# Kernel optimization log

Measured on AMD Instinct MI355X. Metric: run time of the kernel, lower is better.

## Reference

```python
import jax, jax.numpy as jnp
import numpy as np

N_WIRES = 8
N_LAYERS = 6
OUTPUT_DIM = 8
BATCH = 131072


def _rx(t):
    c = jnp.cos(t / 2).astype(jnp.complex64)
    s = jnp.sin(t / 2).astype(jnp.complex64)
    return jnp.stack([jnp.stack([c, -1j * s], -1), jnp.stack([-1j * s, c], -1)], -2)


def _ry(t):
    c = jnp.cos(t / 2).astype(jnp.complex64)
    s = jnp.sin(t / 2).astype(jnp.complex64)
    return jnp.stack([jnp.stack([c, -s], -1), jnp.stack([s, c], -1)], -2)


def _rz(t):
    e = jnp.exp(-0.5j * t.astype(jnp.complex64))
    z = jnp.zeros_like(e)
    return jnp.stack([jnp.stack([e, z], -1), jnp.stack([z, jnp.conj(e)], -1)], -2)


def _apply_1q(state, U, w):
    # state: [B, 2, 2, ..., 2]; U: [2,2] (shared) or [B,2,2] (per-batch angle)
    s = jnp.moveaxis(state, w + 1, -1)
    if U.ndim == 3:
        s = jnp.einsum('bij,b...j->b...i', U, s)
    else:
        s = jnp.einsum('ij,...j->...i', U, s)
    return jnp.moveaxis(s, -1, w + 1)


def _apply_cnot(state, c, t):
    s = jnp.moveaxis(state, (c + 1, t + 1), (-2, -1))
    s = jnp.concatenate([s[..., :1, :], s[..., 1:, ::-1]], axis=-2)
    return jnp.moveaxis(s, (-2, -1), (c + 1, t + 1))


def _circuit(x, weights):
    B = x.shape[0]
    dim = 2 ** N_WIRES
    state = jnp.zeros((B, dim), dtype=jnp.complex64).at[:, 0].set(1.0)
    state = state.reshape((B,) + (2,) * N_WIRES)
    rx0 = _rx(x[:, 0])  # [B,2,2] data-encoding gates (batched angles)
    ry1 = _ry(x[:, 1])
    for layer in range(N_LAYERS):
        for i in range(N_WIRES):
            state = _apply_1q(state, rx0 if i % 2 == 0 else ry1, i)
        for i in range(N_WIRES):
            state = _apply_1q(state, _rx(weights[layer, i, 0]), i)
            state = _apply_1q(state, _ry(weights[layer, i, 1]), i)
            state = _apply_1q(state, _rz(weights[layer, i, 2]), i)
        for i in range(N_WIRES - 1):
            state = _apply_cnot(state, i, i + 1)
    probs = state.real ** 2 + state.imag ** 2  # [B, 2,...,2]
    evs = []
    for i in range(OUTPUT_DIM):
        p = jnp.moveaxis(probs, i + 1, 1).reshape(B, 2, -1)
        evs.append((p[:, 0] - p[:, 1]).sum(-1))  # <Z_i>
    return jnp.stack(evs, 0)  # [output_dim, B]


def setup_inputs() -> dict:
    key = jax.random.key(0)
    k1, k2 = jax.random.split(key)
    x = jax.random.normal(k1, (BATCH, 2), dtype=jnp.float32)
    weights = jax.random.normal(k2, (N_LAYERS, N_WIRES, 3), dtype=jnp.float32)
    return {'x': x, 'weights': weights}


def reference(x, weights):
    basis_t = _circuit(x, weights) * jnp.pi  # [output_dim, B]
    return basis_t.T  # [B, output_dim]
```

## Files before the change

### kernel.cpp

```cpp
#include <hip/hip_runtime.h>
#include <math.h>

#define N_WIRES 8
#define N_LAYERS 6
#define NG 49
#define NG2 (NG * NG)

#define WS_E_OFF 0
#define WS_FB_OFF 76832

typedef _Float16 half8 __attribute__((ext_vector_type(8)));
typedef float f32x4 __attribute__((ext_vector_type(4)));

__global__ __launch_bounds__(256) void qnn_grid_lds(const float* __restrict__ w,
                                                    float* __restrict__ E) {
    __shared__ float gates[N_LAYERS * N_WIRES * 8];
    __shared__ float2 amps[256];
    __shared__ float partial[4][8];

    const int tid = threadIdx.x;
    const int g = blockIdx.x;
    const int ga = (g * 1338) >> 16;
    const int gb = g - ga * NG;
    const float step = (float)(2.0 * M_PI / 49.0);

    if (tid < N_LAYERS * N_WIRES) {
        const int i = tid & 7;
        float wx = w[tid * 3 + 0], wy = w[tid * 3 + 1], wz = w[tid * 3 + 2];
        float sx, cx, sy, cy, sz, cz;
        sincosf(0.5f * wx, &sx, &cx);
        sincosf(0.5f * wy, &sy, &cy);
        sincosf(0.5f * wz, &sz, &cz);
        float A00r = cy * cx, A00i = sy * sx;
        float A01r = -sy * cx, A01i = -cy * sx;
        float A10r = sy * cx, A10i = -cy * sx;
        float A11r = cy * cx, A11i = -sy * sx;
        float U00r = A00r * cz + A00i * sz, U00i = A00i * cz - A00r * sz;
        float U01r = A01r * cz + A01i * sz, U01i = A01i * cz - A01r * sz;
        float U10r = A10r * cz - A10i * sz, U10i = A10i * cz + A10r * sz;
        float U11r = A11r * cz - A11i * sz, U11i = A11i * cz + A11r * sz;
        float V00r, V00i, V01r, V01i, V10r, V10i, V11r, V11i;
        if ((i & 1) == 0) {
            V00r = U01i; V00i = -U01r;
            V01r = U00i; V01i = -U00r;
            V10r = U11i; V10i = -U11r;
            V11r = U10i; V11i = -U10r;
        } else {
            V00r = U01r;  V00i = U01i;
            V01r = -U00r; V01i = -U00i;
            V10r = U11r;  V10i = U11i;
            V11r = -U10r; V11i = -U10i;
        }
        const float xx = (i & 1) ? (step * (float)gb) : (step * (float)ga);
        float se, ce;
        sincosf(0.5f * xx, &se, &ce);
        float* o = gates + tid * 8;
        o[0] = ce * U00r + se * V00r;  o[1] = ce * U00i + se * V00i;
        o[2] = ce * U01r + se * V01r;  o[3] = ce * U01i + se * V01i;
        o[4] = ce * U10r + se * V10r;  o[5] = ce * U10i + se * V10i;
        o[6] = ce * U11r + se * V11r;  o[7] = ce * U11i + se * V11i;
    }

    float ar = (tid == 0) ? 1.0f : 0.0f;
    float ai = 0.0f;
    __syncthreads();

    for (int l = 0; l < N_LAYERS; ++l) {
        #pragma unroll
        for (int i = 0; i < 8; ++i) {
            const float* gm = gates + (l * 8 + i) * 8;
            const int p = 7 - i;
            const int m = 1 << p;
            const int bit = (tid >> p) & 1;
            amps[tid] = make_float2(ar, ai);
            __syncthreads();
            float2 other = amps[tid ^ m];
            float a0r = bit ? other.x : ar, a0i = bit ? other.y : ai;
            float a1r = bit ? ar : other.x, a1i = bit ? ai : other.y;
            float c0r = gm[bit * 4 + 0], c0i = gm[bit * 4 + 1];
            float c1r = gm[bit * 4 + 2], c1i = gm[bit * 4 + 3];
            float nr = c0r * a0r - c0i * a0i + c1r * a1r - c1i * a1i;
            float ni = c0r * a0i + c0i * a0r + c1r * a1i + c1i * a1r;
            __syncthreads();
            ar = nr; ai = ni;
        }
        amps[tid] = make_float2(ar, ai);
        __syncthreads();
        float2 src = amps[tid ^ (tid >> 1)];
        ar = src.x; ai = src.y;
        __syncthreads();
    }

    float p = ar * ar + ai * ai;
    float ev[8];
    #pragma unroll
    for (int i = 0; i < 8; ++i) ev[i] = ((tid >> (7 - i)) & 1) ? -p : p;
    #pragma unroll
    for (int i = 0; i < 8; ++i) {
        #pragma unroll
        for (int s = 1; s < 64; s <<= 1) ev[i] += __shfl_xor(ev[i], s);
    }
    const int wave = tid >> 6, lane = tid & 63;
    if (lane == 0) {
        #pragma unroll
        for (int i = 0; i < 8; ++i) partial[wave][i] = ev[i];
    }
    __syncthreads();
    if (tid < 8) {
        E[tid * NG2 + g] = partial[0][tid] + partial[1][tid] + partial[2][tid] + partial[3][tid];
    }
}

__global__ __launch_bounds__(64) void dft2(const float* __restrict__ E,
                                           _Float16* __restrict__ Fb) {
    const int kp = blockIdx.x, i = blockIdx.y, t = threadIdx.x;
    __shared__ float Es[NG2];
    __shared__ float H[NG];
    const float step = (float)(2.0 * M_PI / 49.0);

    if (kp < NG) {
        for (int e = t; e < NG2; e += 64) Es[e] = E[i * NG2 + e];
    }
    __syncthreads();

    if (kp < NG && t < NG) {
        const int b = t;
        float acc = 0.f;
        if (kp == 0) {
            for (int a = 0; a < NG; ++a) acc += Es[a * NG + b];
            acc *= (1.0f / 49.0f);
        } else {
            const int n = (kp + 1) >> 1;
            float cs, ss;
            sincosf(step * (float)n, &ss, &cs);
            float ca = 1.f, sa = 0.f;
            const bool use_cos = (kp & 1);
            for (int a = 0; a < NG; ++a) {
                acc = fmaf(Es[a * NG + b], use_cos ? ca : sa, acc);
                float cn = ca * cs - sa * ss;
                float sn = sa * cs + ca * ss;
                ca = cn; sa = sn;
            }
            acc *= (2.0f / 49.0f);
        }
        H[b] = acc;
    }
    __syncthreads();

    const int l = t;
    const float PI = 3.14159265358979323846f;
    float acc = 0.f;
    if (kp < NG && l < NG) {
        if (l == 0) {
            for (int b = 0; b < NG; ++b) acc += H[b];
            acc *= (PI / 49.0f);
        } else {
            const int n = (l + 1) >> 1;
            float cs, ss;
            sincosf(step * (float)n, &ss, &cs);
            float cb = 1.f, sb = 0.f;
            const bool use_cos = (l & 1);
            for (int b = 0; b < NG; ++b) {
                acc = fmaf(H[b], use_cos ? cb : sb, acc);
                float cn = cb * cs - sb * ss;
                float sn = sb * cs + cb * ss;
                cb = cn; sb = sn;
            }
            acc *= (2.0f * PI / 49.0f);
        }
    }
    {
        const int ntile = kp >> 4, n = kp & 15;
        const int chunk = l >> 5, lrem = l & 31;
        const int q = lrem >> 3, j = lrem & 7;
        const int fid = (i * 4 + ntile) * 2 + chunk;
        Fb[fid * 512 + (q * 16 + n) * 8 + j] = (_Float16)acc;
    }
}

#define V0PAD 68

__global__ __launch_bounds__(256) void contract_mfma(const float* __restrict__ x,
                                                     const _Float16* __restrict__ Fb,
                                                     float* __restrict__ out, int B) {
    __shared__ float xs0[64], xs1[64];
    __shared__ float v0t[64 * V0PAD];

    const int tid = threadIdx.x;
    const int bbase = blockIdx.x * 64;
    if (bbase >= B) return;

    if (tid < 64) {
        float2 xv = ((const float2*)x)[bbase + tid];
        xs0[tid] = xv.x;
        xs1[tid] = xv.y;
    }
    __syncthreads();

    {
        const int b = tid & 63, s = tid >> 6;
        const float x0 = xs0[b];
        float c1, s1;
        sincosf(x0, &s1, &c1);
        float cb, sb;
        sincosf((float)(8 * s) * x0, &sb, &cb);
        float* row = v0t + b * V0PAD + 16 * s;
        const int k0 = 16 * s;
        row[0] = (k0 == 0) ? 1.0f : ((k0 < NG) ? sb : 0.0f);
        float cm = cb, sm = sb;
        #pragma unroll
        for (int j = 1; j < 16; ++j) {
            if (j & 1) {
                float c2 = cm * c1 - sm * s1, s2 = sm * c1 + cm * s1;
                cm = c2; sm = s2;
            }
            float val = (j & 1) ? cm : sm;
            row[j] = ((k0 + j) < NG) ? val : 0.0f;
        }
    }

    const int lane = tid & 63;
    const int w = tid >> 6;
    const int q = lane >> 4;

    const float x1v = xs1[w * 16 + (lane & 15)];
    float c1, s1;
    sincosf(x1v, &s1, &c1);
    half8 afrag[2];
    #pragma unroll
    for (int c = 0; c < 2; ++c) {
        const int l0 = c * 32 + q * 8;
        float cb, sb;
        sincosf((float)(l0 >> 1) * x1v, &sb, &cb);
        float vals[8];
        vals[0] = (l0 == 0) ? 1.0f : sb;
        float cm = cb, sm = sb;
        #pragma unroll
        for (int j = 1; j < 8; ++j) {
            if (j & 1) {
                float c2 = cm * c1 - sm * s1, s2 = sm * c1 + cm * s1;
                cm = c2; sm = s2;
            }
            vals[j] = (j & 1) ? cm : sm;
        }
        #pragma unroll
        for (int j = 0; j < 8; ++j) {
            afrag[c][j] = (_Float16)(((l0 + j) < 52) ? vals[j] : 0.0f);
        }
    }

    __syncthreads();

    const half8* FB = (const half8*)Fb;

    #pragma unroll 1
    for (int ip = 0; ip < 4; ++ip) {
        const int i0 = ip * 2;

        half8 bfrag[16];
        #pragma unroll
        for (int ii = 0; ii < 2; ++ii)
            #pragma unroll
            for (int nt = 0; nt < 4; ++nt)
                #pragma unroll
                for (int c = 0; c < 2; ++c) {
                    const int fid = ((i0 + ii) * 4 + nt) * 2 + c;
                    bfrag[(ii * 4 + nt) * 2 + c] = FB[fid * 64 + lane];
                }

        f32x4 acc[8];
        #pragma unroll
        for (int t = 0; t < 8; ++t) {
            f32x4 z = {0.f, 0.f, 0.f, 0.f};
            acc[t] = __builtin_amdgcn_mfma_f32_16x16x32_f16(afrag[0], bfrag[t * 2 + 0], z, 0, 0, 0);
            acc[t] = __builtin_amdgcn_mfma_f32_16x16x32_f16(afrag[1], bfrag[t * 2 + 1], acc[t], 0, 0, 0);
        }

        float res[2][4];
        #pragma unroll
        for (int ii = 0; ii < 2; ++ii)
            #pragma unroll
            for (int r = 0; r < 4; ++r) res[ii][r] = 0.f;

        #pragma unroll
        for (int ii = 0; ii < 2; ++ii)
            #pragma unroll
            for (int nt = 0; nt < 4; ++nt) {
                f32x4 a = acc[ii * 4 + nt];
                #pragma unroll
                for (int r = 0; r < 4; ++r) {
                    const int bloc = w * 16 + q * 4 + r;
                    float v0 = v0t[bloc * V0PAD + nt * 16 + (lane & 15)];
                    res[ii][r] = fmaf(a[r], v0, res[ii][r]);
                }
            }

        #pragma unroll
        for (int ii = 0; ii < 2; ++ii)
            #pragma unroll
            for (int r = 0; r < 4; ++r) {
                float v = res[ii][r];
                v += __shfl_xor(v, 1);
                v += __shfl_xor(v, 2);
                v += __shfl_xor(v, 4);
                v += __shfl_xor(v, 8);
                res[ii][r] = v;
            }

        if ((lane & 15) == 0) {
            #pragma unroll
            for (int r = 0; r < 4; ++r) {
                const int b = bbase + w * 16 + q * 4 + r;
                out[(size_t)b * 8 + i0 + 0] = res[0][r];
                out[(size_t)b * 8 + i0 + 1] = res[1][r];
            }
        }
    }
}

extern "C" void kernel_launch(void* const* d_in, const int* in_sizes, int n_in,
                              void* d_out, int out_size, void* d_ws, size_t ws_size,
                              hipStream_t stream) {
    (void)n_in; (void)out_size; (void)ws_size;
    const float* x = (const float*)d_in[0];
    const float* w = (const float*)d_in[1];
    float* out = (float*)d_out;
    char* ws = (char*)d_ws;
    float* E = (float*)(ws + WS_E_OFF);
    _Float16* Fb = (_Float16*)(ws + WS_FB_OFF);
    const int B = in_sizes[0] / 2;

    hipLaunchKernelGGL(qnn_grid_lds, dim3(NG2), dim3(256), 0, stream, w, E);
    hipLaunchKernelGGL(dft2, dim3(64, 8), dim3(64), 0, stream, E, Fb);
    hipLaunchKernelGGL(contract_mfma, dim3((B + 63) / 64, 1), dim3(256), 0, stream,
                       x, Fb, out, B);
}
```

Baseline: 107.7 us.

## Use wave shuffles for low-qubit gates, double-buffer LDS, tabulate DFT twiddles

In the circuit-simulation kernel, gates on the six low-order wires (partner within a 64-lane wave) now use __shfl_xor instead of LDS round trips. The two high wires and the CNOT permutation use alternating LDS buffers, so only one barrier per exchange is needed instead of two. In the DFT kernel, per-thread twiddle recurrences are replaced by a shared sin/cos table indexed modulo 49, which also removes the kp==0 / l==0 special-case branches. This cuts barriers and LDS traffic at the cost of extra shared memory and modular index arithmetic.

```diff
diff --git a/kernel.cpp b/kernel.cpp
--- a/kernel.cpp
+++ b/kernel.cpp
@@ -15,7 +15,8 @@
 __global__ __launch_bounds__(256) void qnn_grid_lds(const float* __restrict__ w,
                                                     float* __restrict__ E) {
     __shared__ float gates[N_LAYERS * N_WIRES * 8];
-    __shared__ float2 amps[256];
+    __shared__ float2 bufA[256];
+    __shared__ float2 bufB[256];
     __shared__ float partial[4][8];
 
     const int tid = threadIdx.x;
@@ -65,30 +66,51 @@
     float ai = 0.0f;
     __syncthreads();
 
+    int flip = 0;
     for (int l = 0; l < N_LAYERS; ++l) {
         #pragma unroll
-        for (int i = 0; i < 8; ++i) {
+        for (int i = 0; i < 2; ++i) {
             const float* gm = gates + (l * 8 + i) * 8;
             const int p = 7 - i;
             const int m = 1 << p;
             const int bit = (tid >> p) & 1;
-            amps[tid] = make_float2(ar, ai);
+            float2* buf = flip ? bufB : bufA;
+            flip ^= 1;
+            buf[tid] = make_float2(ar, ai);
             __syncthreads();
-            float2 other = amps[tid ^ m];
+            float2 other = buf[tid ^ m];
             float a0r = bit ? other.x : ar, a0i = bit ? other.y : ai;
             float a1r = bit ? ar : other.x, a1i = bit ? ai : other.y;
             float c0r = gm[bit * 4 + 0], c0i = gm[bit * 4 + 1];
             float c1r = gm[bit * 4 + 2], c1i = gm[bit * 4 + 3];
             float nr = c0r * a0r - c0i * a0i + c1r * a1r - c1i * a1i;
             float ni = c0r * a0i + c0i * a0r + c1r * a1i + c1i * a1r;
+            ar = nr; ai = ni;
+        }
+        #pragma unroll
+        for (int i = 2; i < 8; ++i) {
+            const float* gm = gates + (l * 8 + i) * 8;
+            const int p = 7 - i;
+            const int m = 1 << p;
+            const int bit = (tid >> p) & 1;
+            float otr = __shfl_xor(ar, m);
+            float oti = __shfl_xor(ai, m);
+            float a0r = bit ? otr : ar, a0i = bit ? oti : ai;
+            float a1r = bit ? ar : otr, a1i = bit ? ai : oti;
+            float c0r = gm[bit * 4 + 0], c0i = gm[bit * 4 + 1];
+            float c1r = gm[bit * 4 + 2], c1i = gm[bit * 4 + 3];
+            float nr = c0r * a0r - c0i * a0i + c1r * a1r - c1i * a1i;
+            float ni = c0r * a0i + c0i * a0r + c1r * a1i + c1i * a1r;
+            ar = nr; ai = ni;
+        }
+        {
+            float2* buf = flip ? bufB : bufA;
+            flip ^= 1;
+            buf[tid] = make_float2(ar, ai);
             __syncthreads();
-            ar = nr; ai = ni;
-        }
-        amps[tid] = make_float2(ar, ai);
-        __syncthreads();
-        float2 src = amps[tid ^ (tid >> 1)];
-        ar = src.x; ai = src.y;
-        __syncthreads();
+            float2 src = buf[tid ^ (tid >> 1)];
+            ar = src.x; ai = src.y;
+        }
     }
 
     float p = ar * ar + ai * ai;
@@ -116,8 +138,15 @@
     const int kp = blockIdx.x, i = blockIdx.y, t = threadIdx.x;
     __shared__ float Es[NG2];
     __shared__ float H[NG];
+    __shared__ float tc[NG], ts[NG];
     const float step = (float)(2.0 * M_PI / 49.0);
-
+    const float PI = 3.14159265358979323846f;
+
+    if (t < NG) {
+        float s, c;
+        sincosf(step * (float)t, &s, &c);
+        tc[t] = c; ts[t] = s;
+    }
     if (kp < NG) {
         for (int e = t; e < NG2; e += 64) Es[e] = E[i * NG2 + e];
     }
@@ -125,49 +154,30 @@
 
     if (kp < NG && t < NG) {
         const int b = t;
+        const int n = (kp + 1) >> 1;
+        const bool use_cos = (kp & 1) || (kp == 0);
         float acc = 0.f;
-        if (kp == 0) {
-            for (int a = 0; a < NG; ++a) acc += Es[a * NG + b];
-            acc *= (1.0f / 49.0f);
-        } else {
-            const int n = (kp + 1) >> 1;
-            float cs, ss;
-            sincosf(step * (float)n, &ss, &cs);
-            float ca = 1.f, sa = 0.f;
-            const bool use_cos = (kp & 1);
-            for (int a = 0; a < NG; ++a) {
-                acc = fmaf(Es[a * NG + b], use_cos ? ca : sa, acc);
-                float cn = ca * cs - sa * ss;
-                float sn = sa * cs + ca * ss;
-                ca = cn; sa = sn;
-            }
-            acc *= (2.0f / 49.0f);
-        }
+        int j = 0;
+        for (int a = 0; a < NG; ++a) {
+            acc = fmaf(Es[a * NG + b], use_cos ? tc[j] : ts[j], acc);
+            j += n; if (j >= NG) j -= NG;
+        }
+        acc *= (kp == 0) ? (1.0f / 49.0f) : (2.0f / 49.0f);
         H[b] = acc;
     }
     __syncthreads();
 
     const int l = t;
-    const float PI = 3.14159265358979323846f;
     float acc = 0.f;
     if (kp < NG && l < NG) {
-        if (l == 0) {
-            for (int b = 0; b < NG; ++b) acc += H[b];
-            acc *= (PI / 49.0f);
-        } else {
-            const int n = (l + 1) >> 1;
-            float cs, ss;
-            sincosf(step * (float)n, &ss, &cs);
-            float cb = 1.f, sb = 0.f;
-            const bool use_cos = (l & 1);
-            for (int b = 0; b < NG; ++b) {
-                acc = fmaf(H[b], use_cos ? cb : sb, acc);
-                float cn = cb * cs - sb * ss;
-                float sn = sb * cs + cb * ss;
-                cb = cn; sb = sn;
-            }
-            acc *= (2.0f * PI / 49.0f);
-        }
+        const int n = (l + 1) >> 1;
+        const bool use_cos = (l & 1) || (l == 0);
+        int j = 0;
+        for (int b = 0; b < NG; ++b) {
+            acc = fmaf(H[b], use_cos ? tc[j] : ts[j], acc);
+            j += n; if (j >= NG) j -= NG;
+        }
+        acc *= (l == 0) ? (PI / 49.0f) : (2.0f * PI / 49.0f);
     }
     {
         const int ntile = kp >> 4, n = kp & 15;
```

Result: no change. 107.0 us (-0.7%).
